# Performance work log

Measured on AMD Instinct MI355X. Metric: run time of the kernel, lower is better.

The kernel has to match this reference:

```python
import jax, jax.numpy as jnp
import numpy as np

B, L, DIN, DT, NOUT = 2, 144, 1024, 150, 4


def setup_inputs() -> dict:
    key = jax.random.key(0)
    ks = jax.random.split(key, 7)
    w = lambda k, shape: (jax.random.normal(k, shape, jnp.float32) * 0.02)
    return dict(
        x=jax.random.normal(ks[0], (B, L, DIN), jnp.float32),
        W_sh=w(ks[1], (DIN, DT)), b_sh=jnp.zeros((DT,), jnp.float32),
        W_st=w(ks[2], (DIN, DT)), b_st=jnp.zeros((DT,), jnp.float32),
        W_oh=w(ks[3], (DIN, DT)), b_oh=jnp.zeros((DT,), jnp.float32),
        W_ot=w(ks[4], (DIN, DT)), b_ot=jnp.zeros((DT,), jnp.float32),
        W_tri1=w(ks[5], (NOUT, DT, DT, DT)),
        W_tri2=w(ks[6], (NOUT, DT, DT, DT)),
    )


def _triaffine(x, y, z, W):
    # supar Triaffine convention: out[b,z,x,y,o] = sum_{i,k,j} x[b,x,i] W[o,i,k,j] y[b,y,j] z[b,z,k]
    w = jnp.einsum('bzk,oikj->bzoij', z, W)      # [B,L,o,d,d]
    t = jnp.einsum('bzoij,byj->bzoiy', w, y)     # [B,L,o,d,L]
    return jnp.einsum('bzoiy,bxi->bzxyo', t, x)  # [B,L,L,L,o]


def reference(x, W_sh, b_sh, W_st, b_st, W_oh, b_oh, W_ot, b_ot, W_tri1, W_tri2):
    # MLP projections (dropout is identity at eval time)
    sh = x @ W_sh + b_sh
    st = x @ W_st + b_st
    oh = x @ W_oh + b_oh
    ot = x @ W_ot + b_ot
    n = x.shape[1]
    # torch .triu() on (..., sh, st) keeps entries with sh <= st, zeros the rest
    tri = jnp.arange(n)[:, None] <= jnp.arange(n)[None, :]
    m = tri[None, :, :, None, None]
    # shstoh = Triaffine(st, rel_oh, sh) -> [b, sh, st, oh, o]; triu over (sh, st)
    s1 = _triaffine(st, oh, sh, W_tri1)
    s1 = jnp.where(m, s1, 0.0)
    # shstot = Triaffine(rel_ot, st, sh) -> [b, sh, ot, st, o]; permutes give (b, sh, st, ot, o) with triu over (sh, st)
    s2 = _triaffine(ot, st, sh, W_tri2)
    s2 = jnp.where(m, jnp.transpose(s2, (0, 1, 3, 2, 4)), 0.0)
    return jax.nn.log_softmax(s1, axis=-1), jax.nn.log_softmax(s2, axis=-1)
```

## Files before the change

kernel.cpp:

```cpp
#include <hip/hip_runtime.h>
#include <hip/hip_bf16.h>
#include <math.h>

typedef unsigned short u16;
typedef __attribute__((ext_vector_type(8))) short bf16x8;
typedef __attribute__((ext_vector_type(4))) float f32x4;

static __device__ __forceinline__ u16 f2bf(float f) {
  __hip_bfloat16 h = __float2bfloat16(f);
  return *reinterpret_cast<u16*>(&h);
}

__global__ __launch_bounds__(256) void conv_x(const float* __restrict__ x,
                                              u16* __restrict__ xb) {
  int idx = (blockIdx.x * 256 + threadIdx.x) * 4;
  float4 v = *(const float4*)(x + idx);
  ushort4 o;
  o.x = f2bf(v.x); o.y = f2bf(v.y); o.z = f2bf(v.z); o.w = f2bf(v.w);
  *(ushort4*)(xb + idx) = o;
}

__global__ __launch_bounds__(256) void trans_wp(
    const float* __restrict__ W0, const float* __restrict__ W1,
    const float* __restrict__ W2, const float* __restrict__ W3,
    u16* __restrict__ WT4) {
  __shared__ float lds[64 * 151];
  int kt = blockIdx.x, p = blockIdx.y;
  const float* W = (p == 0) ? W0 : (p == 1) ? W1 : (p == 2) ? W2 : W3;
  for (int t = threadIdx.x; t < 64 * 150; t += 256) {
    int k = t / 150, j = t - k * 150;
    lds[k * 151 + j] = W[(size_t)(kt * 64 + k) * 150 + j];
  }
  __syncthreads();
  u16* dst = WT4 + (size_t)p * 160 * 1024 + kt * 64;
  for (int t = threadIdx.x; t < 160 * 64; t += 256) {
    int j = t >> 6, kk = t & 63;
    float v = (j < 150) ? lds[kk * 151 + j] : 0.f;
    dst[(size_t)j * 1024 + kk] = f2bf(v);
  }
}

__global__ __launch_bounds__(256) void transw_kernel(
    const float* __restrict__ W, u16* __restrict__ WtT) {
  __shared__ float lds[150 * 151];
  int oi = blockIdx.x;
  const float* src = W + (size_t)oi * 22500;
  for (int t = threadIdx.x; t < 22500; t += 256) {
    int k = t / 150, j = t - k * 150;
    lds[k * 151 + j] = src[t];
  }
  __syncthreads();
  u16* dst = WtT + (size_t)oi * 25600;
  for (int t = threadIdx.x; t < 25600; t += 256) {
    int j = t / 160, k = t - j * 160;
    float v = (j < 150 && k < 150) ? lds[k * 151 + j] : 0.f;
    dst[t] = f2bf(v);
  }
}

template <int STAGE>
__global__ __launch_bounds__(192) void gemm_nt(
    const u16* __restrict__ A, const u16* __restrict__ B, u16* __restrict__ C,
    int Mvalid, int ZcapW, int ZcapT, const float* __restrict__ bias0,
    const float* __restrict__ bias1, const float* __restrict__ bias2,
    const float* __restrict__ bias3) {
  constexpr int BK = (STAGE == 0) ? 128 : 160;
  constexpr int NK = (STAGE == 0) ? 8 : 1;
  constexpr int ST = BK + 8;
  constexpr int C8 = BK / 8;
  constexpr int Astride = (STAGE == 0) ? 1024 : 160;
  constexpr int Bstride = (STAGE == 0) ? 1024 : 160;
  __shared__ __align__(16) u16 lds[224 * ST];
  const u16 *Ab, *Bb;
  u16* Cb = nullptr;
  int cstride = 0;
  if (STAGE == 0) {
    Ab = A + (size_t)blockIdx.y * 144 * 1024;
    Bb = B + (size_t)blockIdx.x * 80 * 1024;
  } else if (STAGE == 1) {
    int b = blockIdx.x, ntile = blockIdx.y, oi = blockIdx.z;
    int o = oi / 150, i = oi - o * 150;
    Ab = A + (size_t)b * 23040;
    Bb = B + (size_t)oi * 25600 + ntile * 12800;
    Cb = C + (size_t)b * ZcapW + ((size_t)o * 160 + i) * 160 + ntile * 80;
    cstride = 102400;
  } else {
    int ntile = blockIdx.x, f2 = blockIdx.y, b = blockIdx.z;
    Ab = A + (size_t)b * 23040;
    Bb = B + (size_t)b * ZcapW + (size_t)f2 * 25600 + ntile * 12800;
    Cb = C + (size_t)b * ZcapT + (size_t)f2 * 23040 + ntile * 80;
    cstride = 160;
  }
  int tid = threadIdx.x;
  int lane = tid & 63, wave = tid >> 6;
  int l16 = lane & 15, quad = lane >> 4;
  f32x4 acc[3][5];
#pragma unroll
  for (int mi = 0; mi < 3; ++mi)
#pragma unroll
    for (int ni = 0; ni < 5; ++ni) acc[mi][ni] = (f32x4){0.f, 0.f, 0.f, 0.f};

  for (int k0 = 0; k0 < NK; ++k0) {
    for (int t = tid; t < 144 * C8; t += 192) {
      int r = t / C8, c = t - r * C8;
      uint4 v = {0u, 0u, 0u, 0u};
      if (r < Mvalid)
        v = *(const uint4*)(Ab + (size_t)r * Astride + k0 * BK + c * 8);
      *(uint4*)&lds[r * ST + c * 8] = v;
    }
    for (int t = tid; t < 80 * C8; t += 192) {
      int r = t / C8, c = t - r * C8;
      uint4 v = *(const uint4*)(Bb + (size_t)r * Bstride + k0 * BK + c * 8);
      *(uint4*)&lds[(144 + r) * ST + c * 8] = v;
    }
    __syncthreads();
    const u16* la = lds + (wave * 48 + l16) * ST + quad * 8;
    const u16* lb = lds + (144 + l16) * ST + quad * 8;
#pragma unroll
    for (int ks = 0; ks < BK / 32; ++ks) {
      bf16x8 af[3], bfr[5];
#pragma unroll
      for (int mi = 0; mi < 3; ++mi)
        af[mi] = *(const bf16x8*)(la + mi * 16 * ST + ks * 32);
#pragma unroll
      for (int ni = 0; ni < 5; ++ni)
        bfr[ni] = *(const bf16x8*)(lb + ni * 16 * ST + ks * 32);
#pragma unroll
      for (int mi = 0; mi < 3; ++mi)
#pragma unroll
        for (int ni = 0; ni < 5; ++ni)
          acc[mi][ni] = __builtin_amdgcn_mfma_f32_16x16x32_bf16(
              af[mi], bfr[ni], acc[mi][ni], 0, 0, 0);
    }
    __syncthreads();
  }

  if (STAGE == 0) {
    int nbase = blockIdx.x * 80;
#pragma unroll
    for (int ni = 0; ni < 5; ++ni) {
      int n = nbase + ni * 16 + l16;
      int p = n / 160, j = n - p * 160;
      const float* bp =
          (p == 0) ? bias0 : (p == 1) ? bias1 : (p == 2) ? bias2 : bias3;
      bool live = (j < 150);
      float bv = live ? bp[j] : 0.f;
#pragma unroll
      for (int mi = 0; mi < 3; ++mi) {
        int row = blockIdx.y * 144 + wave * 48 + mi * 16 + quad * 4;
#pragma unroll
        for (int r = 0; r < 4; ++r) {
          float v = live ? acc[mi][ni][r] + bv : 0.f;
          C[((size_t)p * 288 + row + r) * 160 + j] = f2bf(v);
        }
      }
    }
  } else {
#pragma unroll
    for (int mi = 0; mi < 3; ++mi) {
      int grow0 = wave * 48 + mi * 16 + quad * 4;
#pragma unroll
      for (int ni = 0; ni < 5; ++ni)
#pragma unroll
        for (int r = 0; r < 4; ++r) {
          int grow = grow0 + r;
          if (grow < Mvalid)
            Cb[(size_t)grow * cstride + ni * 16 + l16] = f2bf(acc[mi][ni][r]);
        }
    }
  }
}

template <int VAR>
__global__ __launch_bounds__(256) void stage3_kernel(
    const u16* __restrict__ tb, const u16* __restrict__ P,
    float* __restrict__ out, int z0, int ZcapT) {
  constexpr int ST = 104;
  __shared__ __align__(16) u16 lds[5 * 48 * ST];
  int bx = blockIdx.x;
  int b = bx & 1, xt = (bx >> 1) * 48;
  int yt = blockIdx.y * 48;
  int zl = blockIdx.z;
  int zg = z0 + zl;
  int tid = threadIdx.x;
  const float NL4 = -1.3862943611198906f;
  size_t obase = ((size_t)(b * 144 + zg)) * 82944;
  if (zg > xt + 47) {
    float4 v = make_float4(NL4, NL4, NL4, NL4);
    for (int p = tid; p < 2304; p += 256) {
      int xl = p / 48, yl = p - xl * 48;
      *(float4*)(out + obase + ((size_t)(xt + xl) * 144 + yt + yl) * 4) = v;
    }
    return;
  }
  int pbase = (VAR == 0) ? xt : yt;
  int qbase = (VAR == 0) ? yt : xt;
  const u16* Pb = P + (size_t)b * 23040 + (size_t)pbase * 160;
  const u16* Tz = tb + (size_t)b * ZcapT + (size_t)zl * 92160;
  int lane = tid & 63, o = tid >> 6, l16 = lane & 15, quad = lane >> 4;
  f32x4 acc[3][3];
#pragma unroll
  for (int mi = 0; mi < 3; ++mi)
#pragma unroll
    for (int ni = 0; ni < 3; ++ni) acc[mi][ni] = (f32x4){0.f, 0.f, 0.f, 0.f};

#pragma unroll
  for (int kb = 0; kb < 2; ++kb) {
    const int kbase = kb * 96;
    const int C8 = kb ? 8 : 12;
    for (int t = tid; t < 240 * C8; t += 256) {
      int tile = t / (48 * C8);
      int rr = t - tile * 48 * C8;
      int r = rr / C8, c = rr - r * C8;
      const u16* src =
          (tile == 0)
              ? (Pb + (size_t)r * 160 + kbase + c * 8)
              : (Tz + ((size_t)(tile - 1) * 144 + qbase + r) * 160 + kbase +
                 c * 8);
      *(uint4*)&lds[(tile * 48 + r) * ST + c * 8] = *(const uint4*)src;
    }
    __syncthreads();
    const u16* la;
    const u16* lb;
    if (VAR == 0) {
      la = lds;
      lb = lds + (1 + o) * 48 * ST;
    } else {
      la = lds + (1 + o) * 48 * ST;
      lb = lds;
    }
    const int NKS = kb ? 2 : 3;
#pragma unroll
    for (int ks = 0; ks < 3; ++ks) {
      if (ks >= NKS) break;
      bf16x8 af[3], bfr[3];
#pragma unroll
      for (int mi = 0; mi < 3; ++mi)
        af[mi] = *(const bf16x8*)&la[(mi * 16 + l16) * ST + ks * 32 + quad * 8];
#pragma unroll
      for (int ni = 0; ni < 3; ++ni)
        bfr[ni] =
            *(const bf16x8*)&lb[(ni * 16 + l16) * ST + ks * 32 + quad * 8];
#pragma unroll
      for (int mi = 0; mi < 3; ++mi)
#pragma unroll
        for (int ni = 0; ni < 3; ++ni)
          acc[mi][ni] = __builtin_amdgcn_mfma_f32_16x16x32_bf16(
              af[mi], bfr[ni], acc[mi][ni], 0, 0, 0);
    }
    __syncthreads();
  }

  float* sf = (float*)lds;
#pragma unroll
  for (int mi = 0; mi < 3; ++mi)
#pragma unroll
    for (int ni = 0; ni < 3; ++ni)
#pragma unroll
      for (int r = 0; r < 4; ++r)
        sf[((mi * 16 + quad * 4 + r) * 48 + ni * 16 + l16) * 4 + o] =
            acc[mi][ni][r];
  __syncthreads();
  for (int p = tid; p < 2304; p += 256) {
    int xl = p / 48, yl = p - xl * 48;
    int xg = xt + xl;
    float4 v;
    if (zg > xg) {
      v = make_float4(NL4, NL4, NL4, NL4);
    } else {
      float c0 = sf[p * 4], c1 = sf[p * 4 + 1];
      float c2 = sf[p * 4 + 2], c3 = sf[p * 4 + 3];
      float mx = fmaxf(fmaxf(c0, c1), fmaxf(c2, c3));
      float l = mx + logf(expf(c0 - mx) + expf(c1 - mx) + expf(c2 - mx) +
                          expf(c3 - mx));
      v = make_float4(c0 - l, c1 - l, c2 - l, c3 - l);
    }
    *(float4*)(out + obase + ((size_t)xg * 144 + yt + yl) * 4) = v;
  }
}

extern "C" void kernel_launch(void* const* d_in, const int* in_sizes, int n_in,
                              void* d_out, int out_size, void* d_ws,
                              size_t ws_size, hipStream_t stream) {
  const float* x = (const float*)d_in[0];
  const float* Wsh = (const float*)d_in[1];
  const float* bsh = (const float*)d_in[2];
  const float* Wst = (const float*)d_in[3];
  const float* bst = (const float*)d_in[4];
  const float* Woh = (const float*)d_in[5];
  const float* boh = (const float*)d_in[6];
  const float* Wot = (const float*)d_in[7];
  const float* bot = (const float*)d_in[8];
  const float* Wt1 = (const float*)d_in[9];
  const float* Wt2 = (const float*)d_in[10];

  u16* ws = (u16*)d_ws;
  u16* xb = ws;
  u16* WT4 = ws + 294912;
  u16* pAll = ws + 950272;
  u16* WtT = ws + 1134592;
  u16* dyn = ws + 16494592;
  size_t ws_u = ws_size / 2;
  long long avail = (long long)ws_u - 16494592LL;
  int Zc = (avail > 0) ? (int)(avail / 389120) : 1;
  if (Zc > 144) Zc = 144;
  if (Zc < 1) Zc = 1;
  int ZcapW = Zc * 102400, ZcapT = Zc * 92160;
  u16* wbuf = dyn;
  u16* tbuf = dyn + (size_t)2 * ZcapW;

  conv_x<<<288, 256, 0, stream>>>(x, xb);
  trans_wp<<<dim3(16, 4), 256, 0, stream>>>(Wsh, Wst, Woh, Wot, WT4);
  gemm_nt<0><<<dim3(8, 2), 192, 0, stream>>>(xb, WT4, pAll, 144, 0, 0, bsh,
                                             bst, boh, bot);

  float* out0 = (float*)d_out;
  float* out1 = out0 + 23887872;

  for (int tri = 0; tri < 2; ++tri) {
    transw_kernel<<<600, 256, 0, stream>>>(tri ? Wt2 : Wt1, WtT);
    const u16* shsec = pAll;
    const u16* pQ = pAll + (size_t)(tri ? 1 : 2) * 46080;
    const u16* pP = pAll + (size_t)(tri ? 3 : 1) * 46080;
    float* outT = tri ? out1 : out0;
    for (int z0 = 0; z0 < 144; z0 += Zc) {
      int Zcur = (Zc < 144 - z0) ? Zc : (144 - z0);
      gemm_nt<1><<<dim3(2, 2, 600), 192, 0, stream>>>(
          shsec + (size_t)z0 * 160, WtT, wbuf, Zcur, ZcapW, 0, nullptr,
          nullptr, nullptr, nullptr);
      gemm_nt<2><<<dim3(2, Zcur * 4, 2), 192, 0, stream>>>(
          pQ, wbuf, tbuf, 144, ZcapW, ZcapT, nullptr, nullptr, nullptr,
          nullptr);
      dim3 g3(6, 3, Zcur);
      if (tri == 0)
        stage3_kernel<0><<<g3, 256, 0, stream>>>(tbuf, pP, outT, z0, ZcapT);
      else
        stage3_kernel<1><<<g3, 256, 0, stream>>>(tbuf, pP, outT, z0, ZcapT);
    }
  }
}
```

Measured before the change: 713.4 us.

## Load MFMA fragments directly from global memory, dropping LDS staging in GEMMs

The three GEMM stages and the stage-3 contraction now read bf16 MFMA fragments straight from global memory instead of staging tiles in LDS behind barriers. This removes the LDS round-trip and the `__syncthreads` points, leaving stage3 LDS only for the output transpose. In exchange, fragments shared across waves are fetched repeatedly through the L1/L2 caches with strided 16-byte accesses. The weight transpose kernel is also split across two blocks per slice and now writes 8-element vectors, and the stage-1 grid is reordered so blocks that reuse the same weight slice run close together.

```diff
diff --git a/kernel.cpp b/kernel.cpp
--- a/kernel.cpp
+++ b/kernel.cpp
@@ -4,6 +4,7 @@
 
 typedef unsigned short u16;
 typedef __attribute__((ext_vector_type(8))) short bf16x8;
+typedef __attribute__((ext_vector_type(8))) unsigned short us8;
 typedef __attribute__((ext_vector_type(4))) float f32x4;
 
 static __device__ __forceinline__ u16 f2bf(float f) {
@@ -42,43 +43,51 @@
 
 __global__ __launch_bounds__(256) void transw_kernel(
     const float* __restrict__ W, u16* __restrict__ WtT) {
-  __shared__ float lds[150 * 151];
-  int oi = blockIdx.x;
-  const float* src = W + (size_t)oi * 22500;
-  for (int t = threadIdx.x; t < 22500; t += 256) {
-    int k = t / 150, j = t - k * 150;
-    lds[k * 151 + j] = src[t];
+  __shared__ float lds[150 * 82];
+  int oi = blockIdx.x, jh = blockIdx.y;
+  const float* src = W + (size_t)oi * 22500 + jh * 80;
+  for (int t = threadIdx.x; t < 150 * 40; t += 256) {
+    int k = t / 40, c = t - k * 40;
+    if (jh * 80 + 2 * c < 150) {
+      float2 v = *(const float2*)(src + (size_t)k * 150 + 2 * c);
+      *(float2*)&lds[k * 82 + 2 * c] = v;
+    }
   }
   __syncthreads();
-  u16* dst = WtT + (size_t)oi * 25600;
-  for (int t = threadIdx.x; t < 25600; t += 256) {
-    int j = t / 160, k = t - j * 160;
-    float v = (j < 150 && k < 150) ? lds[k * 151 + j] : 0.f;
-    dst[t] = f2bf(v);
+  u16* dst = WtT + (size_t)oi * 25600 + (size_t)jh * 80 * 160;
+  for (int t = threadIdx.x; t < 80 * 20; t += 256) {
+    int jl = t / 20, kc = t - jl * 20;
+    int j = jh * 80 + jl;
+    bool jlive = (j < 150);
+    us8 v;
+#pragma unroll
+    for (int u = 0; u < 8; ++u) {
+      int k = kc * 8 + u;
+      float f = (jlive && k < 150) ? lds[k * 82 + jl] : 0.f;
+      v[u] = f2bf(f);
+    }
+    *(us8*)(dst + (size_t)jl * 160 + kc * 8) = v;
   }
 }
 
 template <int STAGE>
-__global__ __launch_bounds__(192) void gemm_nt(
+__global__ __launch_bounds__(192) void gemm_ds(
     const u16* __restrict__ A, const u16* __restrict__ B, u16* __restrict__ C,
     int Mvalid, int ZcapW, int ZcapT, const float* __restrict__ bias0,
     const float* __restrict__ bias1, const float* __restrict__ bias2,
     const float* __restrict__ bias3) {
-  constexpr int BK = (STAGE == 0) ? 128 : 160;
-  constexpr int NK = (STAGE == 0) ? 8 : 1;
-  constexpr int ST = BK + 8;
-  constexpr int C8 = BK / 8;
-  constexpr int Astride = (STAGE == 0) ? 1024 : 160;
-  constexpr int Bstride = (STAGE == 0) ? 1024 : 160;
-  __shared__ __align__(16) u16 lds[224 * ST];
+  constexpr int KS = (STAGE == 0) ? 32 : 5;
+  constexpr int AS = (STAGE == 0) ? 1024 : 160;
   const u16 *Ab, *Bb;
   u16* Cb = nullptr;
   int cstride = 0;
+  int mrow0 = 0;
   if (STAGE == 0) {
-    Ab = A + (size_t)blockIdx.y * 144 * 1024;
+    mrow0 = blockIdx.y * 144;
+    Ab = A + (size_t)mrow0 * 1024;
     Bb = B + (size_t)blockIdx.x * 80 * 1024;
   } else if (STAGE == 1) {
-    int b = blockIdx.x, ntile = blockIdx.y, oi = blockIdx.z;
+    int ntile = blockIdx.x, oi = blockIdx.y, b = blockIdx.z;
     int o = oi / 150, i = oi - o * 150;
     Ab = A + (size_t)b * 23040;
     Bb = B + (size_t)oi * 25600 + ntile * 12800;
@@ -94,45 +103,29 @@
   int tid = threadIdx.x;
   int lane = tid & 63, wave = tid >> 6;
   int l16 = lane & 15, quad = lane >> 4;
+  const u16* Ap = Ab + (size_t)(wave * 48 + l16) * AS + quad * 8;
+  const u16* Bp = Bb + (size_t)l16 * AS + quad * 8;
   f32x4 acc[3][5];
 #pragma unroll
   for (int mi = 0; mi < 3; ++mi)
 #pragma unroll
     for (int ni = 0; ni < 5; ++ni) acc[mi][ni] = (f32x4){0.f, 0.f, 0.f, 0.f};
 
-  for (int k0 = 0; k0 < NK; ++k0) {
-    for (int t = tid; t < 144 * C8; t += 192) {
-      int r = t / C8, c = t - r * C8;
-      uint4 v = {0u, 0u, 0u, 0u};
-      if (r < Mvalid)
-        v = *(const uint4*)(Ab + (size_t)r * Astride + k0 * BK + c * 8);
-      *(uint4*)&lds[r * ST + c * 8] = v;
-    }
-    for (int t = tid; t < 80 * C8; t += 192) {
-      int r = t / C8, c = t - r * C8;
-      uint4 v = *(const uint4*)(Bb + (size_t)r * Bstride + k0 * BK + c * 8);
-      *(uint4*)&lds[(144 + r) * ST + c * 8] = v;
-    }
-    __syncthreads();
-    const u16* la = lds + (wave * 48 + l16) * ST + quad * 8;
-    const u16* lb = lds + (144 + l16) * ST + quad * 8;
-#pragma unroll
-    for (int ks = 0; ks < BK / 32; ++ks) {
-      bf16x8 af[3], bfr[5];
-#pragma unroll
-      for (int mi = 0; mi < 3; ++mi)
-        af[mi] = *(const bf16x8*)(la + mi * 16 * ST + ks * 32);
+#pragma unroll
+  for (int ks = 0; ks < KS; ++ks) {
+    bf16x8 af[3], bfr[5];
+#pragma unroll
+    for (int mi = 0; mi < 3; ++mi)
+      af[mi] = *(const bf16x8*)(Ap + (size_t)mi * 16 * AS + ks * 32);
+#pragma unroll
+    for (int ni = 0; ni < 5; ++ni)
+      bfr[ni] = *(const bf16x8*)(Bp + (size_t)ni * 16 * AS + ks * 32);
+#pragma unroll
+    for (int mi = 0; mi < 3; ++mi)
 #pragma unroll
       for (int ni = 0; ni < 5; ++ni)
-        bfr[ni] = *(const bf16x8*)(lb + ni * 16 * ST + ks * 32);
-#pragma unroll
-      for (int mi = 0; mi < 3; ++mi)
-#pragma unroll
-        for (int ni = 0; ni < 5; ++ni)
-          acc[mi][ni] = __builtin_amdgcn_mfma_f32_16x16x32_bf16(
-              af[mi], bfr[ni], acc[mi][ni], 0, 0, 0);
-    }
-    __syncthreads();
+        acc[mi][ni] = __builtin_amdgcn_mfma_f32_16x16x32_bf16(
+            af[mi], bfr[ni], acc[mi][ni], 0, 0, 0);
   }
 
   if (STAGE == 0) {
@@ -147,7 +140,7 @@
       float bv = live ? bp[j] : 0.f;
 #pragma unroll
       for (int mi = 0; mi < 3; ++mi) {
-        int row = blockIdx.y * 144 + wave * 48 + mi * 16 + quad * 4;
+        int row = mrow0 + wave * 48 + mi * 16 + quad * 4;
 #pragma unroll
         for (int r = 0; r < 4; ++r) {
           float v = live ? acc[mi][ni][r] + bv : 0.f;
@@ -175,8 +168,7 @@
 __global__ __launch_bounds__(256) void stage3_kernel(
     const u16* __restrict__ tb, const u16* __restrict__ P,
     float* __restrict__ out, int z0, int ZcapT) {
-  constexpr int ST = 104;
-  __shared__ __align__(16) u16 lds[5 * 48 * ST];
+  __shared__ float sf[9216];
   int bx = blockIdx.x;
   int b = bx & 1, xt = (bx >> 1) * 48;
   int yt = blockIdx.y * 48;
@@ -195,9 +187,12 @@
   }
   int pbase = (VAR == 0) ? xt : yt;
   int qbase = (VAR == 0) ? yt : xt;
-  const u16* Pb = P + (size_t)b * 23040 + (size_t)pbase * 160;
-  const u16* Tz = tb + (size_t)b * ZcapT + (size_t)zl * 92160;
   int lane = tid & 63, o = tid >> 6, l16 = lane & 15, quad = lane >> 4;
+  const u16* Pp = P + (size_t)b * 23040 + (size_t)(pbase + l16) * 160 + quad * 8;
+  const u16* Tp = tb + (size_t)b * ZcapT + (size_t)zl * 92160 +
+                  (size_t)(o * 144 + qbase + l16) * 160 + quad * 8;
+  const u16* Ap = (VAR == 0) ? Pp : Tp;
+  const u16* Bp = (VAR == 0) ? Tp : Pp;
   f32x4 acc[3][3];
 #pragma unroll
   for (int mi = 0; mi < 3; ++mi)
@@ -205,53 +200,22 @@
     for (int ni = 0; ni < 3; ++ni) acc[mi][ni] = (f32x4){0.f, 0.f, 0.f, 0.f};
 
 #pragma unroll
-  for (int kb = 0; kb < 2; ++kb) {
-    const int kbase = kb * 96;
-    const int C8 = kb ? 8 : 12;
-    for (int t = tid; t < 240 * C8; t += 256) {
-      int tile = t / (48 * C8);
-      int rr = t - tile * 48 * C8;
-      int r = rr / C8, c = rr - r * C8;
-      const u16* src =
-          (tile == 0)
-              ? (Pb + (size_t)r * 160 + kbase + c * 8)
-              : (Tz + ((size_t)(tile - 1) * 144 + qbase + r) * 160 + kbase +
-                 c * 8);
-      *(uint4*)&lds[(tile * 48 + r) * ST + c * 8] = *(const uint4*)src;
-    }
-    __syncthreads();
-    const u16* la;
-    const u16* lb;
-    if (VAR == 0) {
-      la = lds;
-      lb = lds + (1 + o) * 48 * ST;
-    } else {
-      la = lds + (1 + o) * 48 * ST;
-      lb = lds;
-    }
-    const int NKS = kb ? 2 : 3;
-#pragma unroll
-    for (int ks = 0; ks < 3; ++ks) {
-      if (ks >= NKS) break;
-      bf16x8 af[3], bfr[3];
-#pragma unroll
-      for (int mi = 0; mi < 3; ++mi)
-        af[mi] = *(const bf16x8*)&la[(mi * 16 + l16) * ST + ks * 32 + quad * 8];
+  for (int ks = 0; ks < 5; ++ks) {
+    bf16x8 af[3], bfr[3];
+#pragma unroll
+    for (int mi = 0; mi < 3; ++mi)
+      af[mi] = *(const bf16x8*)(Ap + (size_t)mi * 16 * 160 + ks * 32);
+#pragma unroll
+    for (int ni = 0; ni < 3; ++ni)
+      bfr[ni] = *(const bf16x8*)(Bp + (size_t)ni * 16 * 160 + ks * 32);
+#pragma unroll
+    for (int mi = 0; mi < 3; ++mi)
 #pragma unroll
       for (int ni = 0; ni < 3; ++ni)
-        bfr[ni] =
-            *(const bf16x8*)&lb[(ni * 16 + l16) * ST + ks * 32 + quad * 8];
-#pragma unroll
-      for (int mi = 0; mi < 3; ++mi)
-#pragma unroll
-        for (int ni = 0; ni < 3; ++ni)
-          acc[mi][ni] = __builtin_amdgcn_mfma_f32_16x16x32_bf16(
-              af[mi], bfr[ni], acc[mi][ni], 0, 0, 0);
-    }
-    __syncthreads();
-  }
-
-  float* sf = (float*)lds;
+        acc[mi][ni] = __builtin_amdgcn_mfma_f32_16x16x32_bf16(
+            af[mi], bfr[ni], acc[mi][ni], 0, 0, 0);
+  }
+
 #pragma unroll
   for (int mi = 0; mi < 3; ++mi)
 #pragma unroll
@@ -311,24 +275,24 @@
 
   conv_x<<<288, 256, 0, stream>>>(x, xb);
   trans_wp<<<dim3(16, 4), 256, 0, stream>>>(Wsh, Wst, Woh, Wot, WT4);
-  gemm_nt<0><<<dim3(8, 2), 192, 0, stream>>>(xb, WT4, pAll, 144, 0, 0, bsh,
+  gemm_ds<0><<<dim3(8, 2), 192, 0, stream>>>(xb, WT4, pAll, 288, 0, 0, bsh,
                                              bst, boh, bot);
 
   float* out0 = (float*)d_out;
   float* out1 = out0 + 23887872;
 
   for (int tri = 0; tri < 2; ++tri) {
-    transw_kernel<<<600, 256, 0, stream>>>(tri ? Wt2 : Wt1, WtT);
+    transw_kernel<<<dim3(600, 2), 256, 0, stream>>>(tri ? Wt2 : Wt1, WtT);
     const u16* shsec = pAll;
     const u16* pQ = pAll + (size_t)(tri ? 1 : 2) * 46080;
     const u16* pP = pAll + (size_t)(tri ? 3 : 1) * 46080;
     float* outT = tri ? out1 : out0;
     for (int z0 = 0; z0 < 144; z0 += Zc) {
       int Zcur = (Zc < 144 - z0) ? Zc : (144 - z0);
-      gemm_nt<1><<<dim3(2, 2, 600), 192, 0, stream>>>(
+      gemm_ds<1><<<dim3(2, 600, 2), 192, 0, stream>>>(
           shsec + (size_t)z0 * 160, WtT, wbuf, Zcur, ZcapW, 0, nullptr,
           nullptr, nullptr, nullptr);
-      gemm_nt<2><<<dim3(2, Zcur * 4, 2), 192, 0, stream>>>(
+      gemm_ds<2><<<dim3(2, Zcur * 4, 2), 192, 0, stream>>>(
           pQ, wbuf, tbuf, 144, ZcapW, ZcapT, nullptr, nullptr, nullptr,
           nullptr);
       dim3 g3(6, 3, Zcur);
```

New measurement: 595.9 us. -16.5%, faster.
